# Optimization experiments

Measured on AMD Instinct MI355X. Metric: run time of the kernel, lower is better.

The kernel has to match this reference:

```python
import jax, jax.numpy as jnp
import numpy as np

N = 4096   # query tokens
M = 4096   # key/value tokens
D = 512    # embedding_dim


def setup_inputs() -> dict:
    key = jax.random.key(0)
    kq, kk, kv = jax.random.split(key, 3)
    return {
        "query": jax.random.normal(kq, (N, D), dtype=jnp.float32),
        "key": jax.random.normal(kk, (M, D), dtype=jnp.float32),
        "value": jax.random.normal(kv, (M, D), dtype=jnp.float32),
    }


def reference(query, key, value):
    # scores = Q K^T  (no 1/sqrt(d) scaling in the original module)
    attention_scores = jnp.einsum("nd,md->nm", query, key)  # [N, M]
    attention_probs = jax.nn.softmax(attention_scores, axis=-1)  # [N, M]
    output = jnp.einsum("nm,md->nd", attention_probs, value)  # [N, D]
    return (output, attention_probs)
```

## Files before the change

kernel.cpp:

```cpp
#include <hip/hip_runtime.h>
#include <hip/hip_bf16.h>
#include <stdint.h>

#define N_Q 4096
#define N_K 4096
#define DIM 512

typedef float f32x4 __attribute__((ext_vector_type(4)));
typedef __bf16 bf16x8 __attribute__((ext_vector_type(8)));
typedef unsigned short u16x4 __attribute__((ext_vector_type(4)));
typedef int i32x4 __attribute__((ext_vector_type(4)));

__device__ __forceinline__ f32x4 mfma_bf16(bf16x8 a, bf16x8 b, f32x4 c) {
  return __builtin_amdgcn_mfma_f32_16x16x32_bf16(a, b, c, 0, 0, 0);
}

__device__ __forceinline__ i32x4 mfma_i8(i32x4 a, i32x4 b, i32x4 c) {
  return __builtin_amdgcn_mfma_i32_16x16x64_i8(a, b, c, 0, 0, 0);
}

__device__ __forceinline__ void gload16(const void* g, void* l) {
  __builtin_amdgcn_global_load_lds((const __attribute__((address_space(1))) void*)g,
                                   (__attribute__((address_space(3))) void*)l,
                                   16, 0, 0);
}

__device__ __forceinline__ void split4(const f32x4 v, u16x4& h, u16x4& l) {
#pragma unroll
  for (int i = 0; i < 4; ++i) {
    float f = v[i];
    uint32_t u = __builtin_bit_cast(uint32_t, f);
    uint32_t hb = (u + 0x8000u) & 0xffff0000u;
    float hf = __builtin_bit_cast(float, hb);
    float lf = f - hf;
    h[i] = (unsigned short)(hb >> 16);
    l[i] = (unsigned short)(__builtin_bit_cast(uint32_t, lf) >> 16);
  }
}

__device__ __forceinline__ unsigned short bf16r(float f) {
  uint32_t u = __builtin_bit_cast(uint32_t, f);
  return (unsigned short)((u + 0x8000u) >> 16);
}

__global__ __launch_bounds__(256) void quant_kernel(const float* __restrict__ Q,
                                                    const float* __restrict__ K,
                                                    signed char* __restrict__ Xq8,
                                                    signed char* __restrict__ Xk8,
                                                    float* __restrict__ sclA,
                                                    float* __restrict__ sclB) {
  const float* X = blockIdx.y ? K : Q;
  signed char* X8 = blockIdx.y ? Xk8 : Xq8;
  float* scl = blockIdx.y ? sclB : sclA;

  const int lane = threadIdx.x & 63;
  const int row = blockIdx.x * 4 + (threadIdx.x >> 6);

  f32x4 v[2];
  v[0] = *(const f32x4*)(X + (size_t)row * DIM + lane * 8);
  v[1] = *(const f32x4*)(X + (size_t)row * DIM + lane * 8 + 4);

  float mx = 0.f;
#pragma unroll
  for (int u = 0; u < 2; ++u)
#pragma unroll
    for (int j = 0; j < 4; ++j) mx = fmaxf(mx, fabsf(v[u][j]));
#pragma unroll
  for (int o = 32; o > 0; o >>= 1) mx = fmaxf(mx, __shfl_xor(mx, o, 64));

  const float s = fmaxf(mx, 1e-20f) * (1.0f / 127.0f);
  const float rinv = 1.0f / s;
  const float linv = 128.0f * rinv;

  uint32_t hw[2], lw[2];
#pragma unroll
  for (int u = 0; u < 2; ++u) {
    uint32_t hword = 0, lword = 0;
#pragma unroll
    for (int j = 0; j < 4; ++j) {
      float x = v[u][j];
      int h = __float2int_rn(x * rinv);
      float r = x - s * (float)h;
      int l = __float2int_rn(r * linv);
      hword |= ((uint32_t)(h & 0xff)) << (8 * j);
      lword |= ((uint32_t)(l & 0xff)) << (8 * j);
    }
    hw[u] = hword; lw[u] = lword;
  }
  uint2 hv; hv.x = hw[0]; hv.y = hw[1];
  uint2 lv; lv.x = lw[0]; lv.y = lw[1];
  *(uint2*)(X8 + (size_t)row * 1024 + lane * 8) = hv;
  *(uint2*)(X8 + (size_t)row * 1024 + 512 + lane * 8) = lv;
  if (lane == 0) scl[row] = s;
}

__global__ __launch_bounds__(256, 2) void qk3_kernel(const signed char* __restrict__ Xq8,
                                                     const signed char* __restrict__ Xk8,
                                                     const float* __restrict__ sclA,
                                                     const float* __restrict__ sclB,
                                                     float* __restrict__ S) {
  __shared__ __align__(16) char smem[65536];

  const int tid = threadIdx.x;
  const int lane = tid & 63, wid = tid >> 6;
  const int wr = wid >> 1, wc = wid & 1;

  const int bid = blockIdx.x;
  const int b = (bid & 7) * 128 + (bid >> 3);
  const int rbase = (b >> 5) * 128;
  const int cbase = (b & 31) * 128;

  const int lrow = lane >> 3;
  const int lchk = lane & 7;

  const i32x4 izero = {0, 0, 0, 0};
  i32x4 acc_hh[4][4], acc_x[4][4];
#pragma unroll
  for (int m = 0; m < 4; ++m)
#pragma unroll
    for (int n = 0; n < 4; ++n) { acc_hh[m][n] = izero; acc_x[m][n] = izero; }

  auto stage = [&](int buf, int t) {
#pragma unroll
    for (int i = 0; i < 4; ++i) {
      const int r = (wid << 5) + (i << 3) + lrow;
      const int sc = lchk ^ (r & 7);
      const int colb = (sc < 4) ? (t * 64 + sc * 16) : (512 + t * 64 + (sc & 3) * 16);
      const signed char* g = Xq8 + (size_t)(rbase + r) * 1024 + colb;
      uint32_t off = (uint32_t)(buf * 32768 + (((wid << 5) + (i << 3)) << 7));
      off = (uint32_t)__builtin_amdgcn_readfirstlane((int)off);
      gload16(g, smem + off);
    }
#pragma unroll
    for (int i = 0; i < 4; ++i) {
      const int r = (wid << 5) + (i << 3) + lrow;
      const int sc = lchk ^ (r & 7);
      const int colb = (sc < 4) ? (t * 64 + sc * 16) : (512 + t * 64 + (sc & 3) * 16);
      const signed char* g = Xk8 + (size_t)(cbase + r) * 1024 + colb;
      uint32_t off = (uint32_t)(buf * 32768 + 16384 + (((wid << 5) + (i << 3)) << 7));
      off = (uint32_t)__builtin_amdgcn_readfirstlane((int)off);
      gload16(g, smem + off);
    }
  };

  auto compute = [&](int buf) {
    const char* bA = smem + buf * 32768;
    const char* bB = bA + 16384;
    const int kc = lane >> 4;
    i32x4 ah[4], al[4], bh[4], bl[4];
#pragma unroll
    for (int m = 0; m < 4; ++m) {
      int row = (wr << 6) + (m << 4) + (lane & 15);
      ah[m] = *(const i32x4*)(bA + row * 128 + ((kc ^ (row & 7)) << 4));
      al[m] = *(const i32x4*)(bA + row * 128 + (((4 + kc) ^ (row & 7)) << 4));
    }
#pragma unroll
    for (int n = 0; n < 4; ++n) {
      int row = (wc << 6) + (n << 4) + (lane & 15);
      bh[n] = *(const i32x4*)(bB + row * 128 + ((kc ^ (row & 7)) << 4));
      bl[n] = *(const i32x4*)(bB + row * 128 + (((4 + kc) ^ (row & 7)) << 4));
    }
#pragma unroll
    for (int m = 0; m < 4; ++m)
#pragma unroll
      for (int n = 0; n < 4; ++n) {
        acc_hh[m][n] = mfma_i8(ah[m], bh[n], acc_hh[m][n]);
        acc_x[m][n]  = mfma_i8(ah[m], bl[n], acc_x[m][n]);
        acc_x[m][n]  = mfma_i8(al[m], bh[n], acc_x[m][n]);
      }
  };

  stage(0, 0);
  __syncthreads();
  int cur = 0;
  for (int t = 0; t < 8; ++t) {
    if (t + 1 < 8) stage(cur ^ 1, t + 1);
    compute(cur);
    __syncthreads();
    cur ^= 1;
  }

#pragma unroll
  for (int m = 0; m < 4; ++m) {
    int row0 = rbase + wr * 64 + m * 16 + (lane >> 4) * 4;
    float sa[4];
#pragma unroll
    for (int j = 0; j < 4; ++j) sa[j] = sclA[row0 + j];
#pragma unroll
    for (int n = 0; n < 4; ++n) {
      int col = cbase + wc * 64 + n * 16 + (lane & 15);
      float sb = sclB[col];
#pragma unroll
      for (int j = 0; j < 4; ++j) {
        float f = (float)acc_hh[m][n][j] + (float)acc_x[m][n][j] * 0.0078125f;
        S[(size_t)(row0 + j) * N_K + col] = sa[j] * sb * f;
      }
    }
  }
}

__global__ __launch_bounds__(256, 2) void qk_kernel(const float* __restrict__ Q,
                                                    const float* __restrict__ K,
                                                    float* __restrict__ S) {
  __shared__ __align__(16) char sAh[16384];
  __shared__ __align__(16) char sAl[16384];
  __shared__ __align__(16) char sBh[16384];
  __shared__ __align__(16) char sBl[16384];

  const int tid = threadIdx.x;
  const int rbase = blockIdx.y * 128;
  const int cbase = blockIdx.x * 128;
  const int lane = tid & 63, wid = tid >> 6;
  const int wr = wid >> 1, wc = wid & 1;
  const int lr = lane & 15, lk = (lane >> 4) * 8;

  const int srow = tid >> 4;
  const int scol = (tid & 15) * 4;

  f32x4 qr[8], kr[8];
#pragma unroll
  for (int p = 0; p < 8; ++p) {
    int r = p * 16 + srow;
    qr[p] = *(const f32x4*)(Q + (size_t)(rbase + r) * DIM + scol);
    kr[p] = *(const f32x4*)(K + (size_t)(cbase + r) * DIM + scol);
  }

  const f32x4 fzero = {0.f, 0.f, 0.f, 0.f};
  f32x4 acc[4][4];
#pragma unroll
  for (int m = 0; m < 4; ++m)
#pragma unroll
    for (int n = 0; n < 4; ++n) acc[m][n] = fzero;

  for (int kk = 0; kk < DIM / 64; ++kk) {
    __syncthreads();
#pragma unroll
    for (int p = 0; p < 8; ++p) {
      int r = p * 16 + srow;
      uint32_t bo = (uint32_t)(r * 128) + (uint32_t)((scol * 2) ^ ((r & 7) << 4));
      u16x4 qh, ql, kh, kl;
      split4(qr[p], qh, ql);
      split4(kr[p], kh, kl);
      *(u16x4*)(sAh + bo) = qh;
      *(u16x4*)(sAl + bo) = ql;
      *(u16x4*)(sBh + bo) = kh;
      *(u16x4*)(sBl + bo) = kl;
    }
    __syncthreads();
    if (kk < DIM / 64 - 1) {
#pragma unroll
      for (int p = 0; p < 8; ++p) {
        int r = p * 16 + srow;
        qr[p] = *(const f32x4*)(Q + (size_t)(rbase + r) * DIM + (kk + 1) * 64 + scol);
        kr[p] = *(const f32x4*)(K + (size_t)(cbase + r) * DIM + (kk + 1) * 64 + scol);
      }
    }
#pragma unroll
    for (int kh = 0; kh < 2; ++kh) {
      bf16x8 a_h[4], a_l[4], b_h[4], b_l[4];
#pragma unroll
      for (int m = 0; m < 4; ++m) {
        int row = wr * 64 + m * 16 + lr;
        uint32_t co = (uint32_t)(((kh * 32 + lk) * 2) ^ ((row & 7) << 4));
        a_h[m] = *(const bf16x8*)(sAh + row * 128 + co);
        a_l[m] = *(const bf16x8*)(sAl + row * 128 + co);
      }
#pragma unroll
      for (int n = 0; n < 4; ++n) {
        int row = wc * 64 + n * 16 + lr;
        uint32_t co = (uint32_t)(((kh * 32 + lk) * 2) ^ ((row & 7) << 4));
        b_h[n] = *(const bf16x8*)(sBh + row * 128 + co);
        b_l[n] = *(const bf16x8*)(sBl + row * 128 + co);
      }
#pragma unroll
      for (int m = 0; m < 4; ++m)
#pragma unroll
        for (int n = 0; n < 4; ++n) {
          acc[m][n] = mfma_bf16(a_h[m], b_h[n], acc[m][n]);
          acc[m][n] = mfma_bf16(a_h[m], b_l[n], acc[m][n]);
          acc[m][n] = mfma_bf16(a_l[m], b_h[n], acc[m][n]);
        }
    }
  }

#pragma unroll
  for (int m = 0; m < 4; ++m) {
    int row = rbase + wr * 64 + m * 16 + (lane >> 4) * 4;
#pragma unroll
    for (int n = 0; n < 4; ++n) {
      int col = cbase + wc * 64 + n * 16 + lr;
#pragma unroll
      for (int j = 0; j < 4; ++j)
        S[(size_t)(row + j) * N_K + col] = acc[m][n][j];
    }
  }
}

__global__ __launch_bounds__(256) void softmax_kernel(float* __restrict__ P,
                                                      unsigned short* __restrict__ Pb) {
  const int tid = threadIdx.x;
  const int wid = tid >> 6, lane = tid & 63;
  float* p = P + (size_t)blockIdx.x * N_K;

  f32x4 v[4];
  float mx = -3.0e38f;
#pragma unroll
  for (int i = 0; i < 4; ++i) {
    v[i] = *(const f32x4*)(p + i * 1024 + tid * 4);
    mx = fmaxf(mx, fmaxf(fmaxf(v[i][0], v[i][1]), fmaxf(v[i][2], v[i][3])));
  }
#pragma unroll
  for (int o = 32; o > 0; o >>= 1) mx = fmaxf(mx, __shfl_xor(mx, o, 64));
  __shared__ float redM[4];
  __shared__ float redS[4];
  if (lane == 0) redM[wid] = mx;
  __syncthreads();
  mx = fmaxf(fmaxf(redM[0], redM[1]), fmaxf(redM[2], redM[3]));

  float s = 0.f;
#pragma unroll
  for (int i = 0; i < 4; ++i) {
#pragma unroll
    for (int j = 0; j < 4; ++j) {
      v[i][j] = __expf(v[i][j] - mx);
      s += v[i][j];
    }
  }
#pragma unroll
  for (int o = 32; o > 0; o >>= 1) s += __shfl_xor(s, o, 64);
  if (lane == 0) redS[wid] = s;
  __syncthreads();
  s = redS[0] + redS[1] + redS[2] + redS[3];
  const float inv = 1.0f / s;

  unsigned short* pb = Pb ? (Pb + (size_t)blockIdx.x * N_K) : nullptr;
#pragma unroll
  for (int i = 0; i < 4; ++i) {
    v[i] *= inv;
    *(f32x4*)(p + i * 1024 + tid * 4) = v[i];
    if (pb) {
      u16x4 h;
#pragma unroll
      for (int j = 0; j < 4; ++j) h[j] = bf16r(v[i][j]);
      *(u16x4*)(pb + i * 1024 + tid * 4) = h;
    }
  }
}

__global__ __launch_bounds__(256) void vt_kernel(const float* __restrict__ V,
                                                 unsigned short* __restrict__ Vt) {
  __shared__ unsigned short t[64][72];
  const int tid = threadIdx.x;
  const int d0 = blockIdx.x * 64;
  const int k0 = blockIdx.y * 64;

#pragma unroll
  for (int c = 0; c < 4; ++c) {
    int kr = (tid >> 4) + c * 16;
    f32x4 v = *(const f32x4*)(V + (size_t)(k0 + kr) * DIM + d0 + (tid & 15) * 4);
#pragma unroll
    for (int j = 0; j < 4; ++j) t[(tid & 15) * 4 + j][kr] = bf16r(v[j]);
  }
  __syncthreads();
#pragma unroll
  for (int c = 0; c < 2; ++c) {
    int d = (tid >> 3) + c * 32;
    int k = (tid & 7) * 8;
    *(uint4*)(Vt + (size_t)(d0 + d) * N_K + k0 + k) = *(const uint4*)&t[d][k];
  }
}

__global__ __launch_bounds__(256, 2) void pv3_kernel(const unsigned short* __restrict__ Pb,
                                                     const unsigned short* __restrict__ Vt,
                                                     float* __restrict__ Opart,
                                                     int kspan) {
  __shared__ __align__(16) char smem[65536];

  const int tid = threadIdx.x;
  const int lane = tid & 63, wid = tid >> 6;
  const int wr = wid >> 1, wc = wid & 1;
  const int rbase = blockIdx.y * 128;
  const int cbase = blockIdx.x * 128;
  const int k0 = blockIdx.z * kspan;
  float* Out = Opart + (size_t)blockIdx.z * ((size_t)N_Q * DIM);

  const int lrow = lane >> 3;
  const int lchk = lane & 7;
  const int iters = kspan >> 6;

  const f32x4 fzero = {0.f, 0.f, 0.f, 0.f};
  f32x4 acc[4][4];
#pragma unroll
  for (int m = 0; m < 4; ++m)
#pragma unroll
    for (int n = 0; n < 4; ++n) acc[m][n] = fzero;

  auto stage = [&](int buf, int t) {
    const size_t kel = (size_t)k0 + ((size_t)t << 6);
#pragma unroll
    for (int i = 0; i < 4; ++i) {
      const int rr = (wid << 5) + (i << 3) + lrow;
      const int gc = lchk ^ (rr & 7);
      const void* gA = (const void*)(Pb + (size_t)(rbase + rr) * N_K + kel + (gc << 3));
      uint32_t off = (uint32_t)(buf * 32768 + (((wid << 5) + (i << 3)) << 7));
      off = (uint32_t)__builtin_amdgcn_readfirstlane((int)off);
      gload16(gA, smem + off);
    }
#pragma unroll
    for (int i = 0; i < 4; ++i) {
      const int rr = (wid << 5) + (i << 3) + lrow;
      const int gc = lchk ^ (rr & 7);
      const void* gB = (const void*)(Vt + (size_t)(cbase + rr) * N_K + kel + (gc << 3));
      uint32_t off = (uint32_t)(buf * 32768 + 16384 + (((wid << 5) + (i << 3)) << 7));
      off = (uint32_t)__builtin_amdgcn_readfirstlane((int)off);
      gload16(gB, smem + off);
    }
  };

  auto compute = [&](int buf) {
    const char* bA = smem + buf * 32768;
    const char* bB = bA + 16384;
#pragma unroll
    for (int kh = 0; kh < 2; ++kh) {
      bf16x8 a[4], b[4];
#pragma unroll
      for (int m = 0; m < 4; ++m) {
        int row = (wr << 6) + (m << 4) + (lane & 15);
        uint32_t co = (uint32_t)(((((kh << 2) + (lane >> 4)) << 4)) ^ ((row & 7) << 4));
        a[m] = *(const bf16x8*)(bA + row * 128 + co);
      }
#pragma unroll
      for (int n = 0; n < 4; ++n) {
        int row = (wc << 6) + (n << 4) + (lane & 15);
        uint32_t co = (uint32_t)(((((kh << 2) + (lane >> 4)) << 4)) ^ ((row & 7) << 4));
        b[n] = *(const bf16x8*)(bB + row * 128 + co);
      }
#pragma unroll
      for (int m = 0; m < 4; ++m)
#pragma unroll
        for (int n = 0; n < 4; ++n)
          acc[m][n] = mfma_bf16(a[m], b[n], acc[m][n]);
    }
  };

  stage(0, 0);
  __syncthreads();
  int cur = 0;
  for (int t = 0; t < iters; ++t) {
    if (t + 1 < iters) stage(cur ^ 1, t + 1);
    compute(cur);
    __syncthreads();
    cur ^= 1;
  }

#pragma unroll
  for (int m = 0; m < 4; ++m) {
    int row = rbase + wr * 64 + m * 16 + (lane >> 4) * 4;
#pragma unroll
    for (int n = 0; n < 4; ++n) {
      int col = cbase + wc * 64 + n * 16 + (lane & 15);
#pragma unroll
      for (int j = 0; j < 4; ++j)
        Out[(size_t)(row + j) * DIM + col] = acc[m][n][j];
    }
  }
}

__global__ __launch_bounds__(256) void reduce_kernel(float* __restrict__ O,
                                                     const float* __restrict__ Opart,
                                                     int nsplit) {
  size_t i = ((size_t)blockIdx.x * 256 + threadIdx.x) * 4;
  f32x4 s = *(const f32x4*)(Opart + i);
  for (int z = 1; z < nsplit; ++z)
    s += *(const f32x4*)(Opart + (size_t)z * ((size_t)N_Q * DIM) + i);
  *(f32x4*)(O + i) = s;
}

__global__ __launch_bounds__(512, 2) void pv_kernel(const float* __restrict__ P,
                                                    const float* __restrict__ V,
                                                    float* __restrict__ O) {
  __shared__ __align__(16) char sA[16384];
  __shared__ __align__(16) char sB[16384];

  const int tid = threadIdx.x;
  const int rbase = blockIdx.y * 128;
  const int cbase = blockIdx.x * 128;
  const int lane = tid & 63, wid = tid >> 6;
  const int wr = wid >> 2, wc = wid & 3;
  const int lr = lane & 15, lk = (lane >> 4) * 8;

  const int a_row = tid >> 4;
  const int a_col = (tid & 15) * 4;
  const int b_c = tid & 127;
  const int b_oct = tid >> 7;

  f32x4 areg[4];
  float breg[4][4];
#pragma unroll
  for (int p = 0; p < 4; ++p) {
    int r = p * 32 + a_row;
    areg[p] = *(const f32x4*)(P + (size_t)(rbase + r) * N_K + a_col);
  }
#pragma unroll
  for (int g = 0; g < 4; ++g) {
    int kr0 = b_oct * 4 + g * 16;
#pragma unroll
    for (int i = 0; i < 4; ++i)
      breg[g][i] = V[(size_t)(kr0 + i) * DIM + cbase + b_c];
  }

  const f32x4 fzero = {0.f, 0.f, 0.f, 0.f};
  f32x4 acc[4][2];
#pragma unroll
  for (int m = 0; m < 4; ++m)
#pragma unroll
    for (int n = 0; n < 2; ++n) acc[m][n] = fzero;

  for (int kk = 0; kk < N_K / 64; ++kk) {
    __syncthreads();
#pragma unroll
    for (int p = 0; p < 4; ++p) {
      int r = p * 32 + a_row;
      uint32_t bo = (uint32_t)(r * 128) + (uint32_t)((a_col * 2) ^ ((r & 7) << 4));
      u16x4 hv;
#pragma unroll
      for (int i = 0; i < 4; ++i) hv[i] = bf16r(areg[p][i]);
      *(u16x4*)(sA + bo) = hv;
    }
#pragma unroll
    for (int g = 0; g < 4; ++g) {
      int kr0 = b_oct * 4 + g * 16;
      uint32_t bo = (uint32_t)(b_c * 128) + (uint32_t)((kr0 * 2) ^ ((b_c & 7) << 4));
      u16x4 hv;
#pragma unroll
      for (int i = 0; i < 4; ++i) hv[i] = bf16r(breg[g][i]);
      *(u16x4*)(sB + bo) = hv;
    }
    __syncthreads();
    if (kk < N_K / 64 - 1) {
#pragma unroll
      for (int p = 0; p < 4; ++p) {
        int r = p * 32 + a_row;
        areg[p] = *(const f32x4*)(P + (size_t)(rbase + r) * N_K + (kk + 1) * 64 + a_col);
      }
#pragma unroll
      for (int g = 0; g < 4; ++g) {
        int kr0 = b_oct * 4 + g * 16;
#pragma unroll
        for (int i = 0; i < 4; ++i)
          breg[g][i] = V[(size_t)((kk + 1) * 64 + kr0 + i) * DIM + cbase + b_c];
      }
    }
#pragma unroll
    for (int kh = 0; kh < 2; ++kh) {
      bf16x8 af[4], bf[2];
#pragma unroll
      for (int m = 0; m < 4; ++m) {
        int row = wr * 64 + m * 16 + lr;
        uint32_t co = (uint32_t)(((kh * 32 + lk) * 2) ^ ((row & 7) << 4));
        af[m] = *(const bf16x8*)(sA + row * 128 + co);
      }
#pragma unroll
      for (int n = 0; n < 2; ++n) {
        int row = wc * 32 + n * 16 + lr;
        uint32_t co = (uint32_t)(((kh * 32 + lk) * 2) ^ ((row & 7) << 4));
        bf[n] = *(const bf16x8*)(sB + row * 128 + co);
      }
#pragma unroll
      for (int m = 0; m < 4; ++m)
#pragma unroll
        for (int n = 0; n < 2; ++n)
          acc[m][n] = mfma_bf16(af[m], bf[n], acc[m][n]);
    }
  }

#pragma unroll
  for (int m = 0; m < 4; ++m) {
    int row = rbase + wr * 64 + m * 16 + (lane >> 4) * 4;
#pragma unroll
    for (int n = 0; n < 2; ++n) {
      int col = cbase + wc * 32 + n * 16 + lr;
#pragma unroll
      for (int j = 0; j < 4; ++j)
        O[(size_t)(row + j) * DIM + col] = acc[m][n][j];
    }
  }
}

extern "C" void kernel_launch(void* const* d_in, const int* in_sizes, int n_in,
                              void* d_out, int out_size, void* d_ws, size_t ws_size,
                              hipStream_t stream) {
  const float* Q = (const float*)d_in[0];
  const float* K = (const float*)d_in[1];
  const float* V = (const float*)d_in[2];
  float* O = (float*)d_out;
  float* P = O + (size_t)N_Q * DIM;

  const size_t PB_BYTES = (size_t)N_Q * N_K * 2;
  const size_t VT_BYTES = (size_t)DIM * N_K * 2;
  const size_t SCL_BYTES = 65536;
  const size_t OP_BYTES = (size_t)N_Q * DIM * 4;

  int nsplit = 0;
  if (ws_size >= PB_BYTES + VT_BYTES + SCL_BYTES + 4 * OP_BYTES) nsplit = 4;
  else if (ws_size >= PB_BYTES + VT_BYTES + SCL_BYTES + 2 * OP_BYTES) nsplit = 2;
  else if (ws_size >= PB_BYTES + VT_BYTES + SCL_BYTES) nsplit = 1;

  if (nsplit > 0) {
    char* wsb = (char*)d_ws;
    signed char* Xq8 = (signed char*)wsb;
    signed char* Xk8 = Xq8 + (size_t)N_Q * 1024;
    unsigned short* Pb = (unsigned short*)wsb;
    unsigned short* Vt = (unsigned short*)(wsb + PB_BYTES);
    float* sclA = (float*)(wsb + PB_BYTES + VT_BYTES);
    float* sclB = sclA + N_Q;
    float* Opart = (float*)(wsb + PB_BYTES + VT_BYTES + SCL_BYTES);

    quant_kernel<<<dim3(N_Q / 4, 2), 256, 0, stream>>>(Q, K, Xq8, Xk8, sclA, sclB);
    vt_kernel<<<dim3(DIM / 64, N_K / 64), 256, 0, stream>>>(V, Vt);
    qk3_kernel<<<1024, 256, 0, stream>>>(Xq8, Xk8, sclA, sclB, P);
    softmax_kernel<<<N_Q, 256, 0, stream>>>(P, Pb);
    if (nsplit == 1) {
      pv3_kernel<<<dim3(DIM / 128, N_Q / 128, 1), 256, 0, stream>>>(Pb, Vt, O, N_K);
    } else {
      pv3_kernel<<<dim3(DIM / 128, N_Q / 128, nsplit), 256, 0, stream>>>(Pb, Vt, Opart, N_K / nsplit);
      reduce_kernel<<<(N_Q * DIM) / (256 * 4), 256, 0, stream>>>(O, Opart, nsplit);
    }
  } else {
    qk_kernel<<<dim3(N_K / 128, N_Q / 128), 256, 0, stream>>>(Q, K, P);
    softmax_kernel<<<N_Q, 256, 0, stream>>>(P, nullptr);
    pv_kernel<<<dim3(DIM / 128, N_Q / 128), 512, 0, stream>>>(P, V, O);
  }
}
```

Baseline: 111.0 us.

## Triple-stage async LDS pipeline with setprio; replace split-K reduce with atomics

Both GEMM kernels (QK int8 and PV bf16) now keep two tiles in flight. They use explicit vmcnt waits and raw s_barrier in place of __syncthreads, and raise wave priority around the MFMA blocks so loads overlap compute better. The PV split-K now always splits into 4 and accumulates into a zeroed output with atomicAdd, replacing the partial buffers and the separate reduce kernel. This drops the workspace requirement and one pass over partial outputs. The cost is atomic contention, nondeterministic summation order, and an extra zero kernel.

```diff
diff --git a/kernel.cpp b/kernel.cpp
--- a/kernel.cpp
+++ b/kernel.cpp
@@ -94,7 +94,7 @@
   if (lane == 0) scl[row] = s;
 }
 
-__global__ __launch_bounds__(256, 2) void qk3_kernel(const signed char* __restrict__ Xq8,
+__global__ __launch_bounds__(256, 2) void qk4_kernel(const signed char* __restrict__ Xq8,
                                                      const signed char* __restrict__ Xk8,
                                                      const float* __restrict__ sclA,
                                                      const float* __restrict__ sclB,
@@ -160,6 +160,7 @@
       bh[n] = *(const i32x4*)(bB + row * 128 + ((kc ^ (row & 7)) << 4));
       bl[n] = *(const i32x4*)(bB + row * 128 + (((4 + kc) ^ (row & 7)) << 4));
     }
+    __builtin_amdgcn_s_setprio(1);
 #pragma unroll
     for (int m = 0; m < 4; ++m)
 #pragma unroll
@@ -168,16 +169,20 @@
         acc_x[m][n]  = mfma_i8(ah[m], bl[n], acc_x[m][n]);
         acc_x[m][n]  = mfma_i8(al[m], bh[n], acc_x[m][n]);
       }
+    __builtin_amdgcn_s_setprio(0);
   };
 
   stage(0, 0);
-  __syncthreads();
-  int cur = 0;
+  stage(1, 1);
   for (int t = 0; t < 8; ++t) {
-    if (t + 1 < 8) stage(cur ^ 1, t + 1);
-    compute(cur);
-    __syncthreads();
-    cur ^= 1;
+    if (t < 7) asm volatile("s_waitcnt vmcnt(8)" ::: "memory");
+    else       asm volatile("s_waitcnt vmcnt(0)" ::: "memory");
+    __builtin_amdgcn_s_barrier();
+    compute(t & 1);
+    asm volatile("s_waitcnt lgkmcnt(0)" ::: "memory");
+    __builtin_amdgcn_sched_barrier(0);
+    __builtin_amdgcn_s_barrier();
+    if (t + 2 < 8) stage(t & 1, t + 2);
   }
 
 #pragma unroll
@@ -370,10 +375,14 @@
   }
 }
 
-__global__ __launch_bounds__(256, 2) void pv3_kernel(const unsigned short* __restrict__ Pb,
+__global__ __launch_bounds__(256) void zero_kernel(float* __restrict__ O) {
+  const f32x4 z = {0.f, 0.f, 0.f, 0.f};
+  *(f32x4*)(O + ((size_t)blockIdx.x * 256 + threadIdx.x) * 4) = z;
+}
+
+__global__ __launch_bounds__(256, 2) void pv4_kernel(const unsigned short* __restrict__ Pb,
                                                      const unsigned short* __restrict__ Vt,
-                                                     float* __restrict__ Opart,
-                                                     int kspan) {
+                                                     float* __restrict__ O) {
   __shared__ __align__(16) char smem[65536];
 
   const int tid = threadIdx.x;
@@ -381,12 +390,10 @@
   const int wr = wid >> 1, wc = wid & 1;
   const int rbase = blockIdx.y * 128;
   const int cbase = blockIdx.x * 128;
-  const int k0 = blockIdx.z * kspan;
-  float* Out = Opart + (size_t)blockIdx.z * ((size_t)N_Q * DIM);
+  const int k0 = blockIdx.z * 1024;
 
   const int lrow = lane >> 3;
   const int lchk = lane & 7;
-  const int iters = kspan >> 6;
 
   const f32x4 fzero = {0.f, 0.f, 0.f, 0.f};
   f32x4 acc[4][4];
@@ -422,7 +429,7 @@
     const char* bB = bA + 16384;
 #pragma unroll
     for (int kh = 0; kh < 2; ++kh) {
-      bf16x8 a[4], b[4];
+      bf16x8 a[4], bfr[4];
 #pragma unroll
       for (int m = 0; m < 4; ++m) {
         int row = (wr << 6) + (m << 4) + (lane & 15);
@@ -433,24 +440,29 @@
       for (int n = 0; n < 4; ++n) {
         int row = (wc << 6) + (n << 4) + (lane & 15);
         uint32_t co = (uint32_t)(((((kh << 2) + (lane >> 4)) << 4)) ^ ((row & 7) << 4));
-        b[n] = *(const bf16x8*)(bB + row * 128 + co);
-      }
+        bfr[n] = *(const bf16x8*)(bB + row * 128 + co);
+      }
+      __builtin_amdgcn_s_setprio(1);
 #pragma unroll
       for (int m = 0; m < 4; ++m)
 #pragma unroll
         for (int n = 0; n < 4; ++n)
-          acc[m][n] = mfma_bf16(a[m], b[n], acc[m][n]);
+          acc[m][n] = mfma_bf16(a[m], bfr[n], acc[m][n]);
+      __builtin_amdgcn_s_setprio(0);
     }
   };
 
   stage(0, 0);
-  __syncthreads();
-  int cur = 0;
-  for (int t = 0; t < iters; ++t) {
-    if (t + 1 < iters) stage(cur ^ 1, t + 1);
-    compute(cur);
-    __syncthreads();
-    cur ^= 1;
+  stage(1, 1);
+  for (int t = 0; t < 16; ++t) {
+    if (t < 15) asm volatile("s_waitcnt vmcnt(8)" ::: "memory");
+    else        asm volatile("s_waitcnt vmcnt(0)" ::: "memory");
+    __builtin_amdgcn_s_barrier();
+    compute(t & 1);
+    asm volatile("s_waitcnt lgkmcnt(0)" ::: "memory");
+    __builtin_amdgcn_sched_barrier(0);
+    __builtin_amdgcn_s_barrier();
+    if (t + 2 < 16) stage(t & 1, t + 2);
   }
 
 #pragma unroll
@@ -461,19 +473,9 @@
       int col = cbase + wc * 64 + n * 16 + (lane & 15);
 #pragma unroll
       for (int j = 0; j < 4; ++j)
-        Out[(size_t)(row + j) * DIM + col] = acc[m][n][j];
-    }
-  }
-}
-
-__global__ __launch_bounds__(256) void reduce_kernel(float* __restrict__ O,
-                                                     const float* __restrict__ Opart,
-                                                     int nsplit) {
-  size_t i = ((size_t)blockIdx.x * 256 + threadIdx.x) * 4;
-  f32x4 s = *(const f32x4*)(Opart + i);
-  for (int z = 1; z < nsplit; ++z)
-    s += *(const f32x4*)(Opart + (size_t)z * ((size_t)N_Q * DIM) + i);
-  *(f32x4*)(O + i) = s;
+        atomicAdd(&O[(size_t)(row + j) * DIM + col], acc[m][n][j]);
+    }
+  }
 }
 
 __global__ __launch_bounds__(512, 2) void pv_kernel(const float* __restrict__ P,
@@ -599,14 +601,8 @@
   const size_t PB_BYTES = (size_t)N_Q * N_K * 2;
   const size_t VT_BYTES = (size_t)DIM * N_K * 2;
   const size_t SCL_BYTES = 65536;
-  const size_t OP_BYTES = (size_t)N_Q * DIM * 4;
-
-  int nsplit = 0;
-  if (ws_size >= PB_BYTES + VT_BYTES + SCL_BYTES + 4 * OP_BYTES) nsplit = 4;
-  else if (ws_size >= PB_BYTES + VT_BYTES + SCL_BYTES + 2 * OP_BYTES) nsplit = 2;
-  else if (ws_size >= PB_BYTES + VT_BYTES + SCL_BYTES) nsplit = 1;
-
-  if (nsplit > 0) {
+
+  if (ws_size >= PB_BYTES + VT_BYTES + SCL_BYTES) {
     char* wsb = (char*)d_ws;
     signed char* Xq8 = (signed char*)wsb;
     signed char* Xk8 = Xq8 + (size_t)N_Q * 1024;
@@ -614,18 +610,13 @@
     unsigned short* Vt = (unsigned short*)(wsb + PB_BYTES);
     float* sclA = (float*)(wsb + PB_BYTES + VT_BYTES);
     float* sclB = sclA + N_Q;
-    float* Opart = (float*)(wsb + PB_BYTES + VT_BYTES + SCL_BYTES);
 
     quant_kernel<<<dim3(N_Q / 4, 2), 256, 0, stream>>>(Q, K, Xq8, Xk8, sclA, sclB);
     vt_kernel<<<dim3(DIM / 64, N_K / 64), 256, 0, stream>>>(V, Vt);
-    qk3_kernel<<<1024, 256, 0, stream>>>(Xq8, Xk8, sclA, sclB, P);
+    qk4_kernel<<<1024, 256, 0, stream>>>(Xq8, Xk8, sclA, sclB, P);
     softmax_kernel<<<N_Q, 256, 0, stream>>>(P, Pb);
-    if (nsplit == 1) {
-      pv3_kernel<<<dim3(DIM / 128, N_Q / 128, 1), 256, 0, stream>>>(Pb, Vt, O, N_K);
-    } else {
-      pv3_kernel<<<dim3(DIM / 128, N_Q / 128, nsplit), 256, 0, stream>>>(Pb, Vt, Opart, N_K / nsplit);
-      reduce_kernel<<<(N_Q * DIM) / (256 * 4), 256, 0, stream>>>(O, Opart, nsplit);
-    }
+    zero_kernel<<<(N_Q * DIM) / (256 * 4), 256, 0, stream>>>(O);
+    pv4_kernel<<<dim3(DIM / 128, N_Q / 128, 4), 256, 0, stream>>>(Pb, Vt, O);
   } else {
     qk_kernel<<<dim3(N_K / 128, N_Q / 128), 256, 0, stream>>>(Q, K, P);
     softmax_kernel<<<N_Q, 256, 0, stream>>>(P, nullptr);
```

After: 129.4 us. +16.6%, slower.
